# Optimization experiments

Hardware: AMD Instinct MI355X
Metric: run time of the kernel (lower is better)

Reference implementation:

```python
import jax, jax.numpy as jnp
import numpy as np

BATCH = 8192
IN_F = 4096
OUT_F = 4096


def setup_inputs() -> dict:
    key = jax.random.key(0)
    k_x, k_w, k_m = jax.random.split(key, 3)
    x = jax.random.normal(k_x, (BATCH, IN_F), dtype=jnp.float32)
    # kaiming_normal_ for relu: std = sqrt(2 / fan_in) with fan_in = in_features
    std = float(np.sqrt(2.0 / IN_F))
    weight = jax.random.normal(k_w, (OUT_F, IN_F), dtype=jnp.float32) * std
    bias = jnp.zeros((OUT_F,), dtype=jnp.float32)
    mask = jax.random.bernoulli(k_m, 0.5, (OUT_F, IN_F)).astype(jnp.float32)
    return {"x": x, "weight": weight, "bias": bias, "mask": mask}


def reference(x, weight, bias, mask):
    # masked_weight = weight * mask; out = x @ masked_weight.T + bias
    masked_weight = weight * mask                      # [out, in]
    return jnp.einsum("bi,oi->bo", x, masked_weight) + bias  # [batch, out]
```

## Files before the change

kernel.cpp:

```cpp
#include <hip/hip_runtime.h>
#include <stdint.h>

#define BATCH 8192
#define IN_F  4096
#define OUT_F 4096

#define BM 256
#define BN 256
#define BK 64
#define KT (IN_F / BK)

typedef __attribute__((ext_vector_type(8))) short bf16x8;
typedef __attribute__((ext_vector_type(4))) float f32x4;


__device__ __forceinline__ unsigned short f2bf(float f) {
    unsigned int u = __float_as_uint(f);
    unsigned int lsb = (u >> 16) & 1u;
    u += 0x7fffu + lsb;
    return (unsigned short)(u >> 16);
}

__device__ __forceinline__ void gl_lds16(const void* g, void* l) {
    __builtin_amdgcn_global_load_lds(
        (const __attribute__((address_space(1))) void*)g,
        (__attribute__((address_space(3))) void*)l,
        16, 0, 0);
}

#define XF4 (BATCH * IN_F / 4)
#define WF4 (OUT_F * IN_F / 4)

__global__ __launch_bounds__(256) void cvt_kernel(const float4* __restrict__ x,
                                                  const float4* __restrict__ w,
                                                  const float4* __restrict__ m,
                                                  uint2* __restrict__ xo,
                                                  uint2* __restrict__ wo) {
    const int i = blockIdx.x * 256 + threadIdx.x;
    union { unsigned short u[4]; uint2 v; } r;
    if (i < XF4) {
        const float4 a = x[i];
        r.u[0] = f2bf(a.x); r.u[1] = f2bf(a.y);
        r.u[2] = f2bf(a.z); r.u[3] = f2bf(a.w);
        xo[i] = r.v;
    } else {
        const int j = i - XF4;
        const float4 a = w[j];
        const float4 b = m[j];
        r.u[0] = f2bf(a.x * b.x); r.u[1] = f2bf(a.y * b.y);
        r.u[2] = f2bf(a.z * b.z); r.u[3] = f2bf(a.w * b.w);
        wo[j] = r.v;
    }
}

__global__ __launch_bounds__(512, 2) void gemm_kernel(const unsigned short* __restrict__ A,
                                                      const unsigned short* __restrict__ W,
                                                      const float* __restrict__ bias,
                                                      float* __restrict__ C) {
    __shared__ unsigned short lA[2][2][128 * BK];
    __shared__ unsigned short lB[2][2][128 * BK];

    const int tid  = threadIdx.x;
    const int lane = tid & 63;
    const int wave = tid >> 6;
    const int wm   = wave >> 2;
    const int wn   = wave & 3;

    const int wg = ((blockIdx.x & 7) << 6) | (blockIdx.x >> 3);
    const int bm = wg >> 4;
    const int bn = wg & 15;

    const int r15 = lane & 15;
    const int g   = lane >> 4;
    const int k0 = (g ^ (r15 & 7)) << 4;

    int hf[4], ldso[4];
    const unsigned short* gA[4];
    const unsigned short* gB[4];
#pragma unroll
    for (int i = 0; i < 4; ++i) {
        const int s    = i * 512 + tid;
        const int h    = s >> 10;
        const int sl   = s & 1023;
        const int row  = sl >> 3;
        const int chnk = (sl & 7) ^ (row & 7);
        hf[i]   = h;
        ldso[i] = sl * 8;
        gA[i] = A + (size_t)(bm * BM + h * 128 + row) * IN_F + chnk * 8;
        gB[i] = W + (size_t)(bn * BN + h * 128 + row) * IN_F + chnk * 8;
    }

#define STAGE_A(buf, ktn)                                               \
    do {                                                                \
        _Pragma("unroll")                                               \
        for (int i = 0; i < 4; ++i)                                     \
            gl_lds16(gA[i] + (ktn) * BK, &lA[buf][hf[i]][ldso[i]]);     \
    } while (0)
#define STAGE_B(buf, ktn)                                               \
    do {                                                                \
        _Pragma("unroll")                                               \
        for (int i = 0; i < 4; ++i)                                     \
            gl_lds16(gB[i] + (ktn) * BK, &lB[buf][hf[i]][ldso[i]]);     \
    } while (0)

    f32x4 acc[8][4] = {};

    STAGE_B(0, 0); STAGE_A(0, 0);
    STAGE_B(1, 1); STAGE_A(1, 1);

    int cur = 0;
    const int brl = (wn & 1) * 64;

    for (int kt = 0; kt < KT; ++kt) {
        if (kt + 1 < KT) { asm volatile("s_waitcnt vmcnt(8)" ::: "memory"); }
        else             { asm volatile("s_waitcnt vmcnt(0)" ::: "memory"); }
        __builtin_amdgcn_sched_barrier(0);
        __builtin_amdgcn_s_barrier();

        const char* aB = (const char*)&lA[cur][wm][0];
        const char* bB = (const char*)&lB[cur][wn >> 1][0];

        bf16x8 bg[4][2], af[2][2];
#pragma unroll
        for (int nf = 0; nf < 4; ++nf)
#pragma unroll
            for (int ks = 0; ks < 2; ++ks)
                bg[nf][ks] = *(const bf16x8*)(bB +
                    ((brl + nf * 16 + r15) << 7) + (k0 ^ (ks << 6)));
#pragma unroll
        for (int i = 0; i < 2; ++i)
#pragma unroll
            for (int ks = 0; ks < 2; ++ks)
                af[i][ks] = *(const bf16x8*)(aB +
                    ((i * 16 + r15) << 7) + (k0 ^ (ks << 6)));
        __builtin_amdgcn_sched_barrier(0);
        __builtin_amdgcn_s_barrier();
        asm volatile("s_waitcnt lgkmcnt(0)" ::: "memory");
        __builtin_amdgcn_sched_barrier(0);

        __builtin_amdgcn_s_setprio(1);
#pragma unroll
        for (int ks = 0; ks < 2; ++ks)
#pragma unroll
            for (int i = 0; i < 2; ++i)
#pragma unroll
                for (int nf = 0; nf < 4; ++nf)
                    acc[i][nf] = __builtin_amdgcn_mfma_f32_16x16x32_bf16(
                        af[i][ks], bg[nf][ks], acc[i][nf], 0, 0, 0);
        __builtin_amdgcn_s_setprio(0);
        __builtin_amdgcn_sched_barrier(0);
        __builtin_amdgcn_s_barrier();

        if (kt + 2 < KT) STAGE_B(cur, kt + 2);
        __builtin_amdgcn_sched_barrier(0);

#pragma unroll
        for (int pp = 1; pp < 4; ++pp) {
#pragma unroll
            for (int i = 0; i < 2; ++i)
#pragma unroll
                for (int ks = 0; ks < 2; ++ks)
                    af[i][ks] = *(const bf16x8*)(aB +
                        ((pp * 32 + i * 16 + r15) << 7) + (k0 ^ (ks << 6)));
            __builtin_amdgcn_sched_barrier(0);
            __builtin_amdgcn_s_barrier();
            asm volatile("s_waitcnt lgkmcnt(0)" ::: "memory");
            __builtin_amdgcn_sched_barrier(0);

            __builtin_amdgcn_s_setprio(1);
#pragma unroll
            for (int ks = 0; ks < 2; ++ks)
#pragma unroll
                for (int i = 0; i < 2; ++i)
#pragma unroll
                    for (int nf = 0; nf < 4; ++nf)
                        acc[pp * 2 + i][nf] = __builtin_amdgcn_mfma_f32_16x16x32_bf16(
                            af[i][ks], bg[nf][ks], acc[pp * 2 + i][nf], 0, 0, 0);
            __builtin_amdgcn_s_setprio(0);
            __builtin_amdgcn_sched_barrier(0);
            __builtin_amdgcn_s_barrier();
        }

        if (kt + 2 < KT) STAGE_A(cur, kt + 2);
        __builtin_amdgcn_sched_barrier(0);
        cur ^= 1;
    }
#undef STAGE_A
#undef STAGE_B

    const int crow0 = bm * BM + wm * 128 + g * 4;
    const int ccol0 = bn * BN + wn * 64 + r15;
#pragma unroll
    for (int nf = 0; nf < 4; ++nf) {
        const int col = ccol0 + nf * 16;
        const float bj = bias[col];
#pragma unroll
        for (int mf = 0; mf < 8; ++mf)
#pragma unroll
            for (int reg = 0; reg < 4; ++reg) {
                const int row = crow0 + mf * 16 + reg;
                C[(size_t)row * OUT_F + col] = acc[mf][nf][reg] + bj;
            }
    }
}

__global__ __launch_bounds__(256) void fallback_kernel(const float* __restrict__ x,
                                                       const float* __restrict__ w,
                                                       const float* __restrict__ bias,
                                                       const float* __restrict__ m,
                                                       float* __restrict__ out) {
    size_t idx = (size_t)blockIdx.x * 256 + threadIdx.x;
    int row = (int)(idx >> 12);
    int col = (int)(idx & (OUT_F - 1));
    const float4* xr = (const float4*)(x + (size_t)row * IN_F);
    const float4* wr = (const float4*)(w + (size_t)col * IN_F);
    const float4* mr = (const float4*)(m + (size_t)col * IN_F);
    float s = 0.f;
    for (int k = 0; k < IN_F / 4; ++k) {
        float4 xv = xr[k], wv = wr[k], mv = mr[k];
        s += xv.x * wv.x * mv.x + xv.y * wv.y * mv.y +
             xv.z * wv.z * mv.z + xv.w * wv.w * mv.w;
    }
    out[idx] = s + bias[col];
}


extern "C" void kernel_launch(void* const* d_in, const int* in_sizes, int n_in,
                              void* d_out, int out_size, void* d_ws, size_t ws_size,
                              hipStream_t stream) {
    const float* x    = (const float*)d_in[0];
    const float* w    = (const float*)d_in[1];
    const float* bias = (const float*)d_in[2];
    const float* mask = (const float*)d_in[3];
    float* out = (float*)d_out;

    const size_t need = ((size_t)BATCH * IN_F + (size_t)OUT_F * IN_F) * sizeof(unsigned short);
    if (ws_size < need) {
        fallback_kernel<<<(size_t)BATCH * OUT_F / 256, 256, 0, stream>>>(
            x, w, bias, mask, out);
        return;
    }

    unsigned short* xb = (unsigned short*)d_ws;
    unsigned short* wb = xb + (size_t)BATCH * IN_F;

    cvt_kernel<<<(XF4 + WF4) / 256, 256, 0, stream>>>(
        (const float4*)x, (const float4*)w, (const float4*)mask,
        (uint2*)xb, (uint2*)wb);

    gemm_kernel<<<512, 512, 0, stream>>>(xb, wb, bias, out);
}
```

Measured before the change: 664.8 us.

## Double-buffer LDS fragment reads in registers across k-halves to overlap with MFMA

The main GEMM loop now splits each BK tile into two k-halves. The A and B fragments for one half are held in registers while the other half's LDS reads are issued under the current half's MFMA block. This cuts the per-iteration barrier and lgkmcnt waits from about eight phases to two, and moves both global-to-LDS stages into a single point. The cost is more VGPRs for two full fragment sets and a vmcnt(0) wait in place of vmcnt(8), which shortens the global prefetch slack.

```diff
diff --git a/kernel.cpp b/kernel.cpp
--- a/kernel.cpp
+++ b/kernel.cpp
@@ -103,90 +103,78 @@
             gl_lds16(gB[i] + (ktn) * BK, &lB[buf][hf[i]][ldso[i]]);     \
     } while (0)
 
+    const int brl = (wn & 1) * 64;
+    const char* aHalf = (const char*)&lA[0][wm][0];
+    const char* bHalf = (const char*)&lB[0][wn >> 1][0];
+
+#define READ_A(dst, curv, ks)                                               \
+    do {                                                                    \
+        _Pragma("unroll")                                                   \
+        for (int mf = 0; mf < 8; ++mf)                                      \
+            dst[mf] = *(const bf16x8*)(aHalf + (curv) * 32768 +             \
+                        ((mf * 16 + r15) << 7) + (k0 ^ ((ks) << 6)));       \
+    } while (0)
+#define READ_B(dst, curv, ks)                                               \
+    do {                                                                    \
+        _Pragma("unroll")                                                   \
+        for (int nf = 0; nf < 4; ++nf)                                      \
+            dst[nf] = *(const bf16x8*)(bHalf + (curv) * 32768 +             \
+                        ((brl + nf * 16 + r15) << 7) + (k0 ^ ((ks) << 6))); \
+    } while (0)
+#define MFMA_ALL(aa, bb)                                                    \
+    do {                                                                    \
+        __builtin_amdgcn_s_setprio(1);                                      \
+        _Pragma("unroll")                                                   \
+        for (int mf = 0; mf < 8; ++mf)                                      \
+            _Pragma("unroll")                                               \
+            for (int nf = 0; nf < 4; ++nf)                                  \
+                acc[mf][nf] = __builtin_amdgcn_mfma_f32_16x16x32_bf16(      \
+                    aa[mf], bb[nf], acc[mf][nf], 0, 0, 0);                  \
+        __builtin_amdgcn_s_setprio(0);                                      \
+    } while (0)
+
     f32x4 acc[8][4] = {};
+    bf16x8 a0[8], b0[4], a1[8], b1[4];
 
     STAGE_B(0, 0); STAGE_A(0, 0);
     STAGE_B(1, 1); STAGE_A(1, 1);
 
+    asm volatile("s_waitcnt vmcnt(8)" ::: "memory");
+    __builtin_amdgcn_s_barrier();
+    __builtin_amdgcn_sched_barrier(0);
+
+    READ_B(b0, 0, 0); READ_A(a0, 0, 0);
+    asm volatile("s_waitcnt lgkmcnt(0)" ::: "memory");
+    __builtin_amdgcn_sched_barrier(0);
+
     int cur = 0;
-    const int brl = (wn & 1) * 64;
-
     for (int kt = 0; kt < KT; ++kt) {
-        if (kt + 1 < KT) { asm volatile("s_waitcnt vmcnt(8)" ::: "memory"); }
-        else             { asm volatile("s_waitcnt vmcnt(0)" ::: "memory"); }
-        __builtin_amdgcn_sched_barrier(0);
-        __builtin_amdgcn_s_barrier();
-
-        const char* aB = (const char*)&lA[cur][wm][0];
-        const char* bB = (const char*)&lB[cur][wn >> 1][0];
-
-        bf16x8 bg[4][2], af[2][2];
-#pragma unroll
-        for (int nf = 0; nf < 4; ++nf)
-#pragma unroll
-            for (int ks = 0; ks < 2; ++ks)
-                bg[nf][ks] = *(const bf16x8*)(bB +
-                    ((brl + nf * 16 + r15) << 7) + (k0 ^ (ks << 6)));
-#pragma unroll
-        for (int i = 0; i < 2; ++i)
-#pragma unroll
-            for (int ks = 0; ks < 2; ++ks)
-                af[i][ks] = *(const bf16x8*)(aB +
-                    ((i * 16 + r15) << 7) + (k0 ^ (ks << 6)));
-        __builtin_amdgcn_sched_barrier(0);
-        __builtin_amdgcn_s_barrier();
+        READ_B(b1, cur, 1); READ_A(a1, cur, 1);
+        MFMA_ALL(a0, b0);
         asm volatile("s_waitcnt lgkmcnt(0)" ::: "memory");
         __builtin_amdgcn_sched_barrier(0);
 
-        __builtin_amdgcn_s_setprio(1);
-#pragma unroll
-        for (int ks = 0; ks < 2; ++ks)
-#pragma unroll
-            for (int i = 0; i < 2; ++i)
-#pragma unroll
-                for (int nf = 0; nf < 4; ++nf)
-                    acc[i][nf] = __builtin_amdgcn_mfma_f32_16x16x32_bf16(
-                        af[i][ks], bg[nf][ks], acc[i][nf], 0, 0, 0);
-        __builtin_amdgcn_s_setprio(0);
-        __builtin_amdgcn_sched_barrier(0);
-        __builtin_amdgcn_s_barrier();
-
-        if (kt + 2 < KT) STAGE_B(cur, kt + 2);
-        __builtin_amdgcn_sched_barrier(0);
-
-#pragma unroll
-        for (int pp = 1; pp < 4; ++pp) {
-#pragma unroll
-            for (int i = 0; i < 2; ++i)
-#pragma unroll
-                for (int ks = 0; ks < 2; ++ks)
-                    af[i][ks] = *(const bf16x8*)(aB +
-                        ((pp * 32 + i * 16 + r15) << 7) + (k0 ^ (ks << 6)));
+        if (kt + 1 < KT) {
+            asm volatile("s_waitcnt vmcnt(0)" ::: "memory");
+            __builtin_amdgcn_s_barrier();
             __builtin_amdgcn_sched_barrier(0);
-            __builtin_amdgcn_s_barrier();
+
+            const int nxt = cur ^ 1;
+            READ_B(b0, nxt, 0); READ_A(a0, nxt, 0);
+            if (kt + 2 < KT) { STAGE_B(cur, kt + 2); STAGE_A(cur, kt + 2); }
+            MFMA_ALL(a1, b1);
             asm volatile("s_waitcnt lgkmcnt(0)" ::: "memory");
             __builtin_amdgcn_sched_barrier(0);
-
-            __builtin_amdgcn_s_setprio(1);
-#pragma unroll
-            for (int ks = 0; ks < 2; ++ks)
-#pragma unroll
-                for (int i = 0; i < 2; ++i)
-#pragma unroll
-                    for (int nf = 0; nf < 4; ++nf)
-                        acc[pp * 2 + i][nf] = __builtin_amdgcn_mfma_f32_16x16x32_bf16(
-                            af[i][ks], bg[nf][ks], acc[pp * 2 + i][nf], 0, 0, 0);
-            __builtin_amdgcn_s_setprio(0);
-            __builtin_amdgcn_sched_barrier(0);
-            __builtin_amdgcn_s_barrier();
+            cur = nxt;
+        } else {
+            MFMA_ALL(a1, b1);
         }
-
-        if (kt + 2 < KT) STAGE_A(cur, kt + 2);
-        __builtin_amdgcn_sched_barrier(0);
-        cur ^= 1;
     }
 #undef STAGE_A
 #undef STAGE_B
+#undef READ_A
+#undef READ_B
+#undef MFMA_ALL
 
     const int crow0 = bm * BM + wm * 128 + g * 4;
     const int ccol0 = bn * BN + wn * 64 + r15;
```

Measured after the change: 582.5 us. 12.4% less time.
